# Performance work log

Measured on AMD Instinct MI355X. Metric: run time of the kernel, lower is better.

Reference implementation:

```python
import jax, jax.numpy as jnp
import numpy as np

D_MODEL = 1024
N_HEAD = 16
HEAD_DIM = D_MODEL // N_HEAD


def setup_inputs() -> dict:
    key = jax.random.key(0)
    k1, k2, k3 = jax.random.split(key, 3)
    B, T = 2, 2048
    x = jax.random.normal(k1, (B, T, D_MODEL), dtype=jnp.float32)
    # nn.MultiheadAttention packed in-projection: (3*D, D), xavier-like scale
    w_in = jax.random.normal(k2, (3 * D_MODEL, D_MODEL), dtype=jnp.float32) * (1.0 / np.sqrt(D_MODEL))
    b_in = jnp.zeros((3 * D_MODEL,), dtype=jnp.float32)
    w_out = jax.random.normal(k3, (D_MODEL, D_MODEL), dtype=jnp.float32) * (1.0 / np.sqrt(D_MODEL))
    b_out = jnp.zeros((D_MODEL,), dtype=jnp.float32)
    return {"x": x, "w_in": w_in, "b_in": b_in, "w_out": w_out, "b_out": b_out}


def reference(x, w_in, b_in, w_out, b_out):
    B, T, D = x.shape
    H, hd = N_HEAD, HEAD_DIM
    # packed QKV projection (torch Linear convention: y = x @ W.T + b)
    qkv = x @ w_in.T + b_in                      # [B, T, 3D]
    q, k, v = jnp.split(qkv, 3, axis=-1)
    # [B, H, T, hd]
    q = q.reshape(B, T, H, hd).transpose(0, 2, 1, 3)
    k = k.reshape(B, T, H, hd).transpose(0, 2, 1, 3)
    v = v.reshape(B, T, H, hd).transpose(0, 2, 1, 3)
    scale = 1.0 / np.sqrt(hd).astype(np.float32)
    scores = jnp.einsum("bhqd,bhkd->bhqk", q * scale, k)  # [B, H, T, T]
    causal = jnp.tril(jnp.ones((T, T), dtype=bool))
    scores = jnp.where(causal, scores, jnp.finfo(scores.dtype).min)
    attn = jax.nn.softmax(scores, axis=-1)
    ctx = jnp.einsum("bhqk,bhkd->bhqd", attn, v)           # [B, H, T, hd]
    ctx = ctx.transpose(0, 2, 1, 3).reshape(B, T, D)
    return ctx @ w_out.T + b_out
```

## Files before the change

### kernel.cpp

```cpp
#include <hip/hip_runtime.h>


#define T_SEQ 2048
#define D_MODEL 1024
#define NEG_BIG (-1.0e30f)
#define Q_SCALE 0.18033688f

typedef float f32x4 __attribute__((ext_vector_type(4)));
typedef short s16x8 __attribute__((ext_vector_type(8)));
typedef __bf16 bf16x8 __attribute__((ext_vector_type(8)));

__device__ __forceinline__ f32x4 mfma16(s16x8 a, s16x8 b, f32x4 c) {
    return __builtin_amdgcn_mfma_f32_16x16x32_bf16(
        __builtin_bit_cast(bf16x8, a), __builtin_bit_cast(bf16x8, b), c, 0, 0, 0);
}

__device__ __forceinline__ short f2bf(float f) {
    unsigned int u = __float_as_uint(f);
    u += 0x7fffu + ((u >> 16) & 1u);
    return (short)(u >> 16);
}
__device__ __forceinline__ unsigned f2bfu(float f) {
    unsigned int u = __float_as_uint(f);
    u += 0x7fffu + ((u >> 16) & 1u);
    return u >> 16;
}
__device__ __forceinline__ unsigned f2bfu_fast(float f) {
    return (__float_as_uint(f) + 0x8000u) >> 16;
}
__device__ __forceinline__ float bf2f(short s) {
    return __uint_as_float(((unsigned int)(unsigned short)s) << 16);
}

__device__ __forceinline__ void async_lds16(const short* g, short* l) {
    __builtin_amdgcn_global_load_lds(
        (const __attribute__((address_space(1))) unsigned int*)g,
        (__attribute__((address_space(3))) unsigned int*)l, 16, 0, 0);
}

#define N_X   4194304
#define N_WI  3145728
#define N_BI  3072
#define N_WO  1048576
#define N_BO  1024
#define V_X   (N_X  / 4)
#define V_WI  (N_WI / 4)
#define V_BI  (N_BI / 4)
#define V_WO  (N_WO / 4)
#define V_BO  (N_BO / 4)
#define V_TOT (V_X + V_WI + V_BI + V_WO + V_BO)

__global__ __launch_bounds__(256) void canon_all_kernel(
    const float* __restrict__ x, const float* __restrict__ wi,
    const float* __restrict__ bi, const float* __restrict__ wo,
    const float* __restrict__ bo,
    short* __restrict__ xb, short* __restrict__ wib, short* __restrict__ bib,
    short* __restrict__ wob, short* __restrict__ bob)
{
    int i = blockIdx.x * 256 + threadIdx.x;
    if (i >= V_TOT) return;
    const float* src; short* dst; int off;
    if      (i < V_X)                    { src = x;  dst = xb;  off = i; }
    else if (i < V_X+V_WI)               { src = wi; dst = wib; off = i - V_X; }
    else if (i < V_X+V_WI+V_BI)          { src = bi; dst = bib; off = i - V_X - V_WI; }
    else if (i < V_X+V_WI+V_BI+V_WO)     { src = wo; dst = wob; off = i - V_X - V_WI - V_BI; }
    else                                 { src = bo; dst = bob; off = i - V_X - V_WI - V_BI - V_WO; }
    float4 v = ((const float4*)src)[off];
    short4 o = { f2bf(v.x), f2bf(v.y), f2bf(v.z), f2bf(v.w) };
    ((short4*)dst)[off] = o;
}

__global__ __launch_bounds__(256) void gemm_qkv_kernel(
    const short* __restrict__ A, const short* __restrict__ B,
    const short* __restrict__ bias,
    short* __restrict__ qo, short* __restrict__ ko, short* __restrict__ vo)
{
    const int K = 1024;
    alignas(16) __shared__ short As[128][32];
    alignas(16) __shared__ short Bs[128][32];
    const int m0 = blockIdx.x * 128;
    const int n0 = blockIdx.y * 128;
    const int tid = threadIdx.x;
    const int lane = tid & 63;
    const int w = tid >> 6;
    const int wm = (w >> 1) * 64, wn = (w & 1) * 64;
    const int quad = lane >> 4, l16 = lane & 15;

    f32x4 acc[4][4];
    const f32x4 zero = {0.f, 0.f, 0.f, 0.f};
#pragma unroll
    for (int i = 0; i < 4; ++i)
#pragma unroll
        for (int j = 0; j < 4; ++j) acc[i][j] = zero;

    const int lrow = lane >> 2;
    const int lcol = (lane & 3) * 8;
    const short* gA0 = &A[(m0 + w*32      + lrow) * K + lcol];
    const short* gA1 = &A[(m0 + w*32 + 16 + lrow) * K + lcol];
    const short* gB0 = &B[(n0 + w*32      + lrow) * K + lcol];
    const short* gB1 = &B[(n0 + w*32 + 16 + lrow) * K + lcol];
    short* lA0 = &As[w*32][0];
    short* lA1 = &As[w*32 + 16][0];
    short* lB0 = &Bs[w*32][0];
    short* lB1 = &Bs[w*32 + 16][0];

    for (int k0 = 0; k0 < K; k0 += 32) {
        __syncthreads();
        async_lds16(gA0 + k0, lA0);
        async_lds16(gA1 + k0, lA1);
        async_lds16(gB0 + k0, lB0);
        async_lds16(gB1 + k0, lB1);
        __syncthreads();

        s16x8 af[4], bfr[4];
#pragma unroll
        for (int i = 0; i < 4; ++i) af[i]  = *(const s16x8*)&As[wm + i*16 + l16][quad*8];
#pragma unroll
        for (int j = 0; j < 4; ++j) bfr[j] = *(const s16x8*)&Bs[wn + j*16 + l16][quad*8];
#pragma unroll
        for (int i = 0; i < 4; ++i)
#pragma unroll
            for (int j = 0; j < 4; ++j)
                acc[i][j] = mfma16(af[i], bfr[j], acc[i][j]);
    }

#pragma unroll
    for (int j = 0; j < 4; ++j) {
        int n = n0 + wn + j*16 + l16;
        float bi = bf2f(bias[n]);
        int which = n >> 10;
        short* dst = (which == 0) ? qo : (which == 1) ? ko : vo;
        float scl = (which == 0) ? Q_SCALE : 1.0f;
        int h = (n >> 6) & 15, d = n & 63;
#pragma unroll
        for (int i = 0; i < 4; ++i) {
#pragma unroll
            for (int r = 0; r < 4; ++r) {
                int m = m0 + wm + i*16 + quad*4 + r;
                int b = m >> 11, t = m & 2047;
                float v = (acc[i][j][r] + bi) * scl;
                dst[(((b*16 + h) * 2048) + t) * 64 + d] = f2bf(v);
            }
        }
    }
}

__global__ __launch_bounds__(256) void transpose_v_kernel(
    const short* __restrict__ V, short* __restrict__ Vt)
{
    alignas(16) __shared__ short buf[64][72];
    const int bh = blockIdx.x;
    const int t0 = blockIdx.y * 64;
    const int tid = threadIdx.x;
    const int r = tid >> 2;
    const int c = (tid & 3) * 16;

    const short* src = V + ((size_t)bh * T_SEQ + t0) * 64;
    *(float4*)&buf[r][c]     = *(const float4*)&src[r * 64 + c];
    *(float4*)&buf[r][c + 8] = *(const float4*)&src[r * 64 + c + 8];
    __syncthreads();

    s16x8 o0, o1;
#pragma unroll
    for (int k2 = 0; k2 < 8; ++k2) {
        o0[k2] = buf[c + k2][r];
        o1[k2] = buf[c + 8 + k2][r];
    }
    short* dst = Vt + ((size_t)bh * 64 + r) * T_SEQ + t0;
    *(s16x8*)&dst[c]     = o0;
    *(s16x8*)&dst[c + 8] = o1;
}

__global__ __launch_bounds__(256) void attn_kernel(
    const short* __restrict__ Q, const short* __restrict__ K,
    const short* __restrict__ Vt, short* __restrict__ ctx)
{
    alignas(16) __shared__ short Ks[64][72];
    alignas(16) __shared__ short Vs[64][72];
    alignas(16) __shared__ short Pl[4][16][72];

    const int bh = blockIdx.x;
    const int qt = 31 - (int)blockIdx.y;
    const int qbase = qt * 64;
    const int tid = threadIdx.x;
    const int w = tid >> 6, lane = tid & 63;
    const int quad = lane >> 4, l16 = lane & 15;
    const int b = bh >> 4, h = bh & 15;

    const short* Qb  = Q  + bh * T_SEQ * 64;
    const short* Kb  = K  + bh * T_SEQ * 64;
    const short* Vbt = Vt + (size_t)bh * 64 * T_SEQ;

    const short* qrow = Qb + (qbase + w*16 + l16) * 64;
    const s16x8 qa0 = *(const s16x8*)(qrow + quad*8);
    const s16x8 qa1 = *(const s16x8*)(qrow + 32 + quad*8);

    const f32x4 zero = {0.f, 0.f, 0.f, 0.f};
    f32x4 o[4];
#pragma unroll
    for (int dt = 0; dt < 4; ++dt) o[dt] = zero;
    float lsum = 0.f;

    const int sr  = tid >> 3;
    const int scl = (tid & 7) * 8;
    const int qg  = qbase + w*16 + l16;

    float4 kf0 = *(const float4*)&Kb[sr * 64 + scl];
    float4 kf1 = *(const float4*)&Kb[(sr + 32) * 64 + scl];
    float4 vf0 = *(const float4*)&Vbt[(size_t)sr * T_SEQ + scl];
    float4 vf1 = *(const float4*)&Vbt[(size_t)(sr + 32) * T_SEQ + scl];

    for (int s0 = 0; s0 <= qbase; s0 += 64) {
        __syncthreads();
        *(float4*)&Ks[sr][scl]    = kf0;
        *(float4*)&Ks[sr+32][scl] = kf1;
        *(float4*)&Vs[sr][scl]    = vf0;
        *(float4*)&Vs[sr+32][scl] = vf1;
        __syncthreads();

        if (s0 + 64 <= qbase) {
            kf0 = *(const float4*)&Kb[(s0 + 64 + sr) * 64 + scl];
            kf1 = *(const float4*)&Kb[(s0 + 64 + sr + 32) * 64 + scl];
            vf0 = *(const float4*)&Vbt[(size_t)sr * T_SEQ + s0 + 64 + scl];
            vf1 = *(const float4*)&Vbt[(size_t)(sr + 32) * T_SEQ + s0 + 64 + scl];
        }

#pragma unroll
        for (int sub = 0; sub < 4; ++sub) {
            s16x8 ka0 = *(const s16x8*)&Ks[sub*16 + l16][quad*8];
            s16x8 ka1 = *(const s16x8*)&Ks[sub*16 + l16][32 + quad*8];
            f32x4 S = mfma16(ka1, qa1, mfma16(ka0, qa0, zero));
            if (s0 == qbase) {
                int sb = s0 + sub*16 + quad*4;
#pragma unroll
                for (int r = 0; r < 4; ++r)
                    if (sb + r > qg) S[r] = NEG_BIG;
            }
            float p0 = exp2f(S[0]), p1 = exp2f(S[1]);
            float p2 = exp2f(S[2]), p3 = exp2f(S[3]);
            lsum += (p0 + p1) + (p2 + p3);
            uint2 pk;
            pk.x = f2bfu_fast(p0) | (f2bfu_fast(p1) << 16);
            pk.y = f2bfu_fast(p2) | (f2bfu_fast(p3) << 16);
            *(uint2*)&Pl[w][l16][sub*16 + quad*4] = pk;
        }

        s16x8 pb0 = *(const s16x8*)&Pl[w][l16][quad*8];
        s16x8 pb1 = *(const s16x8*)&Pl[w][l16][32 + quad*8];
#pragma unroll
        for (int dt = 0; dt < 4; ++dt) {
            s16x8 va0 = *(const s16x8*)&Vs[dt*16 + l16][quad*8];
            s16x8 va1 = *(const s16x8*)&Vs[dt*16 + l16][32 + quad*8];
            o[dt] = mfma16(va1, pb1, mfma16(va0, pb0, o[dt]));
        }
    }

    lsum += __shfl_xor(lsum, 16, 64);
    lsum += __shfl_xor(lsum, 32, 64);
    float inv = 1.0f / lsum;
    int base = (b * T_SEQ + qg) * D_MODEL + h * 64;
#pragma unroll
    for (int dt = 0; dt < 4; ++dt) {
        uint2 pk;
        pk.x = f2bfu(o[dt][0] * inv) | (f2bfu(o[dt][1] * inv) << 16);
        pk.y = f2bfu(o[dt][2] * inv) | (f2bfu(o[dt][3] * inv) << 16);
        *(uint2*)&ctx[base + dt*16 + quad*4] = pk;
    }
}

__global__ __launch_bounds__(256) void gemm_out_kernel(
    const short* __restrict__ A, const short* __restrict__ B,
    const short* __restrict__ bias, float* __restrict__ out)
{
    const int K = 1024;
    alignas(16) __shared__ short As[128][32];
    alignas(16) __shared__ short Bs[64][32];
    const int m0 = blockIdx.x * 128;
    const int n0 = blockIdx.y * 64;
    const int tid = threadIdx.x;
    const int lane = tid & 63;
    const int w = tid >> 6;
    const int wm = (w >> 1) * 64, wn = (w & 1) * 32;
    const int quad = lane >> 4, l16 = lane & 15;

    f32x4 acc[4][2];
    const f32x4 zero = {0.f, 0.f, 0.f, 0.f};
#pragma unroll
    for (int i = 0; i < 4; ++i)
#pragma unroll
        for (int j = 0; j < 2; ++j) acc[i][j] = zero;

    const int lrow = lane >> 2;
    const int lcol = (lane & 3) * 8;
    const short* gA0 = &A[(m0 + w*32      + lrow) * K + lcol];
    const short* gA1 = &A[(m0 + w*32 + 16 + lrow) * K + lcol];
    const short* gB0 = &B[(n0 + w*16 + lrow) * K + lcol];
    short* lA0 = &As[w*32][0];
    short* lA1 = &As[w*32 + 16][0];
    short* lB0 = &Bs[w*16][0];

    for (int k0 = 0; k0 < K; k0 += 32) {
        __syncthreads();
        async_lds16(gA0 + k0, lA0);
        async_lds16(gA1 + k0, lA1);
        async_lds16(gB0 + k0, lB0);
        __syncthreads();

        s16x8 af[4], bfr[2];
#pragma unroll
        for (int i = 0; i < 4; ++i) af[i]  = *(const s16x8*)&As[wm + i*16 + l16][quad*8];
#pragma unroll
        for (int j = 0; j < 2; ++j) bfr[j] = *(const s16x8*)&Bs[wn + j*16 + l16][quad*8];
#pragma unroll
        for (int i = 0; i < 4; ++i)
#pragma unroll
            for (int j = 0; j < 2; ++j)
                acc[i][j] = mfma16(af[i], bfr[j], acc[i][j]);
    }

#pragma unroll
    for (int j = 0; j < 2; ++j) {
        int n = n0 + wn + j*16 + l16;
        float bi = bf2f(bias[n]);
#pragma unroll
        for (int i = 0; i < 4; ++i) {
#pragma unroll
            for (int r = 0; r < 4; ++r) {
                int m = m0 + wm + i*16 + quad*4 + r;
                out[m * 1024 + n] = acc[i][j][r] + bi;
            }
        }
    }
}

extern "C" void kernel_launch(void* const* d_in, const int* in_sizes, int n_in,
                              void* d_out, int out_size, void* d_ws, size_t ws_size,
                              hipStream_t stream) {
    float* out = (float*)d_out;
    char* ws = (char*)d_ws;

    const size_t MB = 1u << 20;
    short* xb     = (short*)(ws);
    short* w_inb  = (short*)(ws + 8*MB);
    short* b_inb  = (short*)(ws + 14*MB);
    short* w_outb = (short*)(ws + 15*MB);
    short* b_outb = (short*)(ws + 17*MB);
    short* qb     = (short*)(ws + 18*MB);
    short* kb     = (short*)(ws + 26*MB);
    short* vb     = (short*)(ws + 34*MB);
    short* ctxb   = (short*)(ws + 42*MB);
    short* vtb    = xb;

    canon_all_kernel<<<(V_TOT + 255) / 256, 256, 0, stream>>>(
        (const float*)d_in[0], (const float*)d_in[1], (const float*)d_in[2],
        (const float*)d_in[3], (const float*)d_in[4],
        xb, w_inb, b_inb, w_outb, b_outb);

    gemm_qkv_kernel<<<dim3(32, 24), 256, 0, stream>>>(xb, w_inb, b_inb, qb, kb, vb);
    transpose_v_kernel<<<dim3(32, 32), 256, 0, stream>>>(vb, vtb);
    attn_kernel<<<dim3(32, 32), 256, 0, stream>>>(qb, kb, vtb, ctxb);
    gemm_out_kernel<<<dim3(32, 16), 256, 0, stream>>>(ctxb, w_outb, b_outb, out);
}
```

Baseline: 178.4 us.

## Pair short and long causal query tiles per attention block for load balance

Each attention workgroup now handles two query tiles, j and 31-j, sharing the same K/V tiles loaded into shared memory, and the grid is halved in y. This evens out the causal triangle's work across blocks and halves K/V loads for the shorter tile. In exchange it doubles accumulator registers and adds a second P buffer in shared memory, which may lower occupancy, and leaves half as many blocks to fill the GPU.

```diff
diff --git a/kernel.cpp b/kernel.cpp
--- a/kernel.cpp
+++ b/kernel.cpp
@@ -177,11 +177,13 @@
 {
     alignas(16) __shared__ short Ks[64][72];
     alignas(16) __shared__ short Vs[64][72];
-    alignas(16) __shared__ short Pl[4][16][72];
+    alignas(16) __shared__ short PlA[4][16][72];
+    alignas(16) __shared__ short PlB[4][16][72];
 
     const int bh = blockIdx.x;
-    const int qt = 31 - (int)blockIdx.y;
-    const int qbase = qt * 64;
+    const int j  = blockIdx.y;
+    const int qbaseA = j * 64;
+    const int qbaseB = (31 - j) * 64;
     const int tid = threadIdx.x;
     const int w = tid >> 6, lane = tid & 63;
     const int quad = lane >> 4, l16 = lane & 15;
@@ -191,26 +193,30 @@
     const short* Kb  = K  + bh * T_SEQ * 64;
     const short* Vbt = Vt + (size_t)bh * 64 * T_SEQ;
 
-    const short* qrow = Qb + (qbase + w*16 + l16) * 64;
-    const s16x8 qa0 = *(const s16x8*)(qrow + quad*8);
-    const s16x8 qa1 = *(const s16x8*)(qrow + 32 + quad*8);
+    const int qgA = qbaseA + w*16 + l16;
+    const int qgB = qbaseB + w*16 + l16;
+    const short* qrowA = Qb + qgA * 64;
+    const short* qrowB = Qb + qgB * 64;
+    const s16x8 qaA0 = *(const s16x8*)(qrowA + quad*8);
+    const s16x8 qaA1 = *(const s16x8*)(qrowA + 32 + quad*8);
+    const s16x8 qaB0 = *(const s16x8*)(qrowB + quad*8);
+    const s16x8 qaB1 = *(const s16x8*)(qrowB + 32 + quad*8);
 
     const f32x4 zero = {0.f, 0.f, 0.f, 0.f};
-    f32x4 o[4];
-#pragma unroll
-    for (int dt = 0; dt < 4; ++dt) o[dt] = zero;
-    float lsum = 0.f;
+    f32x4 oA[4], oB[4];
+#pragma unroll
+    for (int dt = 0; dt < 4; ++dt) { oA[dt] = zero; oB[dt] = zero; }
+    float lsumA = 0.f, lsumB = 0.f;
 
     const int sr  = tid >> 3;
     const int scl = (tid & 7) * 8;
-    const int qg  = qbase + w*16 + l16;
 
     float4 kf0 = *(const float4*)&Kb[sr * 64 + scl];
     float4 kf1 = *(const float4*)&Kb[(sr + 32) * 64 + scl];
     float4 vf0 = *(const float4*)&Vbt[(size_t)sr * T_SEQ + scl];
     float4 vf1 = *(const float4*)&Vbt[(size_t)(sr + 32) * T_SEQ + scl];
 
-    for (int s0 = 0; s0 <= qbase; s0 += 64) {
+    for (int s0 = 0; s0 <= qbaseB; s0 += 64) {
         __syncthreads();
         *(float4*)&Ks[sr][scl]    = kf0;
         *(float4*)&Ks[sr+32][scl] = kf1;
@@ -218,53 +224,89 @@
         *(float4*)&Vs[sr+32][scl] = vf1;
         __syncthreads();
 
-        if (s0 + 64 <= qbase) {
+        if (s0 + 64 <= qbaseB) {
             kf0 = *(const float4*)&Kb[(s0 + 64 + sr) * 64 + scl];
             kf1 = *(const float4*)&Kb[(s0 + 64 + sr + 32) * 64 + scl];
             vf0 = *(const float4*)&Vbt[(size_t)sr * T_SEQ + s0 + 64 + scl];
             vf1 = *(const float4*)&Vbt[(size_t)(sr + 32) * T_SEQ + s0 + 64 + scl];
         }
 
+        const bool doA = (s0 <= qbaseA);
+
 #pragma unroll
         for (int sub = 0; sub < 4; ++sub) {
             s16x8 ka0 = *(const s16x8*)&Ks[sub*16 + l16][quad*8];
             s16x8 ka1 = *(const s16x8*)&Ks[sub*16 + l16][32 + quad*8];
-            f32x4 S = mfma16(ka1, qa1, mfma16(ka0, qa0, zero));
-            if (s0 == qbase) {
+
+            f32x4 SB = mfma16(ka1, qaB1, mfma16(ka0, qaB0, zero));
+            if (s0 == qbaseB) {
                 int sb = s0 + sub*16 + quad*4;
 #pragma unroll
                 for (int r = 0; r < 4; ++r)
-                    if (sb + r > qg) S[r] = NEG_BIG;
+                    if (sb + r > qgB) SB[r] = NEG_BIG;
             }
-            float p0 = exp2f(S[0]), p1 = exp2f(S[1]);
-            float p2 = exp2f(S[2]), p3 = exp2f(S[3]);
-            lsum += (p0 + p1) + (p2 + p3);
-            uint2 pk;
-            pk.x = f2bfu_fast(p0) | (f2bfu_fast(p1) << 16);
-            pk.y = f2bfu_fast(p2) | (f2bfu_fast(p3) << 16);
-            *(uint2*)&Pl[w][l16][sub*16 + quad*4] = pk;
-        }
-
-        s16x8 pb0 = *(const s16x8*)&Pl[w][l16][quad*8];
-        s16x8 pb1 = *(const s16x8*)&Pl[w][l16][32 + quad*8];
+            {
+                float p0 = exp2f(SB[0]), p1 = exp2f(SB[1]);
+                float p2 = exp2f(SB[2]), p3 = exp2f(SB[3]);
+                lsumB += (p0 + p1) + (p2 + p3);
+                uint2 pk;
+                pk.x = f2bfu_fast(p0) | (f2bfu_fast(p1) << 16);
+                pk.y = f2bfu_fast(p2) | (f2bfu_fast(p3) << 16);
+                *(uint2*)&PlB[w][l16][sub*16 + quad*4] = pk;
+            }
+
+            if (doA) {
+                f32x4 SA = mfma16(ka1, qaA1, mfma16(ka0, qaA0, zero));
+                if (s0 == qbaseA) {
+                    int sb = s0 + sub*16 + quad*4;
+#pragma unroll
+                    for (int r = 0; r < 4; ++r)
+                        if (sb + r > qgA) SA[r] = NEG_BIG;
+                }
+                float p0 = exp2f(SA[0]), p1 = exp2f(SA[1]);
+                float p2 = exp2f(SA[2]), p3 = exp2f(SA[3]);
+                lsumA += (p0 + p1) + (p2 + p3);
+                uint2 pk;
+                pk.x = f2bfu_fast(p0) | (f2bfu_fast(p1) << 16);
+                pk.y = f2bfu_fast(p2) | (f2bfu_fast(p3) << 16);
+                *(uint2*)&PlA[w][l16][sub*16 + quad*4] = pk;
+            }
+        }
+
+        s16x8 pbB0 = *(const s16x8*)&PlB[w][l16][quad*8];
+        s16x8 pbB1 = *(const s16x8*)&PlB[w][l16][32 + quad*8];
+        s16x8 pbA0, pbA1;
+        if (doA) {
+            pbA0 = *(const s16x8*)&PlA[w][l16][quad*8];
+            pbA1 = *(const s16x8*)&PlA[w][l16][32 + quad*8];
+        }
 #pragma unroll
         for (int dt = 0; dt < 4; ++dt) {
             s16x8 va0 = *(const s16x8*)&Vs[dt*16 + l16][quad*8];
             s16x8 va1 = *(const s16x8*)&Vs[dt*16 + l16][32 + quad*8];
-            o[dt] = mfma16(va1, pb1, mfma16(va0, pb0, o[dt]));
-        }
-    }
-
-    lsum += __shfl_xor(lsum, 16, 64);
-    lsum += __shfl_xor(lsum, 32, 64);
-    float inv = 1.0f / lsum;
-    int base = (b * T_SEQ + qg) * D_MODEL + h * 64;
+            oB[dt] = mfma16(va1, pbB1, mfma16(va0, pbB0, oB[dt]));
+            if (doA)
+                oA[dt] = mfma16(va1, pbA1, mfma16(va0, pbA0, oA[dt]));
+        }
+    }
+
+    lsumB += __shfl_xor(lsumB, 16, 64);
+    lsumB += __shfl_xor(lsumB, 32, 64);
+    lsumA += __shfl_xor(lsumA, 16, 64);
+    lsumA += __shfl_xor(lsumA, 32, 64);
+    float invB = 1.0f / lsumB;
+    float invA = 1.0f / lsumA;
+    int baseB = (b * T_SEQ + qgB) * D_MODEL + h * 64;
+    int baseA = (b * T_SEQ + qgA) * D_MODEL + h * 64;
 #pragma unroll
     for (int dt = 0; dt < 4; ++dt) {
         uint2 pk;
-        pk.x = f2bfu(o[dt][0] * inv) | (f2bfu(o[dt][1] * inv) << 16);
-        pk.y = f2bfu(o[dt][2] * inv) | (f2bfu(o[dt][3] * inv) << 16);
-        *(uint2*)&ctx[base + dt*16 + quad*4] = pk;
+        pk.x = f2bfu(oB[dt][0] * invB) | (f2bfu(oB[dt][1] * invB) << 16);
+        pk.y = f2bfu(oB[dt][2] * invB) | (f2bfu(oB[dt][3] * invB) << 16);
+        *(uint2*)&ctx[baseB + dt*16 + quad*4] = pk;
+        pk.x = f2bfu(oA[dt][0] * invA) | (f2bfu(oA[dt][1] * invA) << 16);
+        pk.y = f2bfu(oA[dt][2] * invA) | (f2bfu(oA[dt][3] * invA) << 16);
+        *(uint2*)&ctx[baseA + dt*16 + quad*4] = pk;
     }
 }
 
@@ -358,6 +400,6 @@
 
     gemm_qkv_kernel<<<dim3(32, 24), 256, 0, stream>>>(xb, w_inb, b_inb, qb, kb, vb);
     transpose_v_kernel<<<dim3(32, 32), 256, 0, stream>>>(vb, vtb);
-    attn_kernel<<<dim3(32, 32), 256, 0, stream>>>(qb, kb, vtb, ctxb);
+    attn_kernel<<<dim3(32, 16), 256, 0, stream>>>(qb, kb, vtb, ctxb);
     gemm_out_kernel<<<dim3(32, 16), 256, 0, stream>>>(ctxb, w_outb, b_outb, out);
 }
```

Measured after the change: 183.3 us. +2.7%, slower.

## Fuse V transpose into QKV GEMM epilogue and rebalance attention block order

Applied to the files above, without the earlier changes.

The QKV GEMM epilogue now writes V directly in transposed [bh][d][t] layout with 4-wide vector stores, which removes the separate transpose kernel launch and its extra global round trip. The attention grid becomes 1-D with a custom block-to-(head, q-tile) mapping. That mapping interleaves short and long causal q-tiles across head groups to balance load across CUs. The trade-off is that the strided transposed stores in the epilogue are less coalesced.

```diff
diff --git a/kernel.cpp b/kernel.cpp
--- a/kernel.cpp
+++ b/kernel.cpp
@@ -73,7 +73,7 @@
 __global__ __launch_bounds__(256) void gemm_qkv_kernel(
     const short* __restrict__ A, const short* __restrict__ B,
     const short* __restrict__ bias,
-    short* __restrict__ qo, short* __restrict__ ko, short* __restrict__ vo)
+    short* __restrict__ qo, short* __restrict__ ko, short* __restrict__ vto)
 {
     const int K = 1024;
     alignas(16) __shared__ short As[128][32];
@@ -129,46 +129,31 @@
         int n = n0 + wn + j*16 + l16;
         float bi = bf2f(bias[n]);
         int which = n >> 10;
-        short* dst = (which == 0) ? qo : (which == 1) ? ko : vo;
-        float scl = (which == 0) ? Q_SCALE : 1.0f;
         int h = (n >> 6) & 15, d = n & 63;
-#pragma unroll
-        for (int i = 0; i < 4; ++i) {
-#pragma unroll
-            for (int r = 0; r < 4; ++r) {
-                int m = m0 + wm + i*16 + quad*4 + r;
-                int b = m >> 11, t = m & 2047;
-                float v = (acc[i][j][r] + bi) * scl;
-                dst[(((b*16 + h) * 2048) + t) * 64 + d] = f2bf(v);
+        if (which < 2) {
+            short* dst = (which == 0) ? qo : ko;
+            float scl = (which == 0) ? Q_SCALE : 1.0f;
+#pragma unroll
+            for (int i = 0; i < 4; ++i) {
+#pragma unroll
+                for (int r = 0; r < 4; ++r) {
+                    int m = m0 + wm + i*16 + quad*4 + r;
+                    int b = m >> 11, t = m & 2047;
+                    float v = (acc[i][j][r] + bi) * scl;
+                    dst[(((b*16 + h) * 2048) + t) * 64 + d] = f2bf(v);
+                }
             }
-        }
-    }
-}
-
-__global__ __launch_bounds__(256) void transpose_v_kernel(
-    const short* __restrict__ V, short* __restrict__ Vt)
-{
-    alignas(16) __shared__ short buf[64][72];
-    const int bh = blockIdx.x;
-    const int t0 = blockIdx.y * 64;
-    const int tid = threadIdx.x;
-    const int r = tid >> 2;
-    const int c = (tid & 3) * 16;
-
-    const short* src = V + ((size_t)bh * T_SEQ + t0) * 64;
-    *(float4*)&buf[r][c]     = *(const float4*)&src[r * 64 + c];
-    *(float4*)&buf[r][c + 8] = *(const float4*)&src[r * 64 + c + 8];
-    __syncthreads();
-
-    s16x8 o0, o1;
-#pragma unroll
-    for (int k2 = 0; k2 < 8; ++k2) {
-        o0[k2] = buf[c + k2][r];
-        o1[k2] = buf[c + 8 + k2][r];
-    }
-    short* dst = Vt + ((size_t)bh * 64 + r) * T_SEQ + t0;
-    *(s16x8*)&dst[c]     = o0;
-    *(s16x8*)&dst[c + 8] = o1;
+        } else {
+#pragma unroll
+            for (int i = 0; i < 4; ++i) {
+                int m = m0 + wm + i*16 + quad*4;
+                int b = m >> 11, t0 = m & 2047;
+                short4 o4 = { f2bf(acc[i][j][0] + bi), f2bf(acc[i][j][1] + bi),
+                              f2bf(acc[i][j][2] + bi), f2bf(acc[i][j][3] + bi) };
+                *(short4*)&vto[(((size_t)(b*16 + h) * 64) + d) * 2048 + t0] = o4;
+            }
+        }
+    }
 }
 
 __global__ __launch_bounds__(256) void attn_kernel(
@@ -179,8 +164,17 @@
     alignas(16) __shared__ short Vs[64][72];
     alignas(16) __shared__ short Pl[4][16][72];
 
-    const int bh = blockIdx.x;
-    const int qt = 31 - (int)blockIdx.y;
+    const int id = blockIdx.x;
+    const int kk = id >> 8;
+    const int r8 = id & 255;
+    const int a  = r8 & 15;
+    const int bhl = r8 >> 4;
+    int qt, bh;
+    if      (kk == 0) { qt = a;      bh = bhl;      }
+    else if (kk == 1) { qt = 31 - a; bh = bhl;      }
+    else if (kk == 2) { qt = 15 - a; bh = 16 + bhl; }
+    else              { qt = 16 + a; bh = 16 + bhl; }
+
     const int qbase = qt * 64;
     const int tid = threadIdx.x;
     const int w = tid >> 6, lane = tid & 63;
@@ -347,17 +341,15 @@
     short* b_outb = (short*)(ws + 17*MB);
     short* qb     = (short*)(ws + 18*MB);
     short* kb     = (short*)(ws + 26*MB);
-    short* vb     = (short*)(ws + 34*MB);
+    short* vtb    = (short*)(ws + 34*MB);
     short* ctxb   = (short*)(ws + 42*MB);
-    short* vtb    = xb;
 
     canon_all_kernel<<<(V_TOT + 255) / 256, 256, 0, stream>>>(
         (const float*)d_in[0], (const float*)d_in[1], (const float*)d_in[2],
         (const float*)d_in[3], (const float*)d_in[4],
         xb, w_inb, b_inb, w_outb, b_outb);
 
-    gemm_qkv_kernel<<<dim3(32, 24), 256, 0, stream>>>(xb, w_inb, b_inb, qb, kb, vb);
-    transpose_v_kernel<<<dim3(32, 32), 256, 0, stream>>>(vb, vtb);
-    attn_kernel<<<dim3(32, 32), 256, 0, stream>>>(qb, kb, vtb, ctxb);
+    gemm_qkv_kernel<<<dim3(32, 24), 256, 0, stream>>>(xb, w_inb, b_inb, qb, kb, vtb);
+    attn_kernel<<<dim3(1024), 256, 0, stream>>>(qb, kb, vtb, ctxb);
     gemm_out_kernel<<<dim3(32, 16), 256, 0, stream>>>(ctxb, w_outb, b_outb, out);
 }
```

Result: slower. 184.2 us (+3.3%).
